# Performance work log

Hardware: AMD Instinct MI355X
Metric: run time of the kernel (lower is better)

## Reference

```python
import jax, jax.numpy as jnp
import numpy as np

N_NODES, F_IN, HID, HEADS, REP, NCLS = 8192, 128, 64, 8, 512, 32
E, NSYN, LMAX = 2048, 4096, 8
DM, DI, DSTATE, DCONV, DTR = 512, 1024, 16, 4, 32


def setup_inputs():
    key = jax.random.key(0)
    ks = jax.random.split(key, 24)
    g = lambda i, shape, s=0.05: jax.random.normal(ks[i], shape, jnp.float32) * s
    return {
        "edge_attr": jax.random.normal(ks[0], (E, 8), jnp.float32),
        "synapse": jax.random.normal(ks[1], (NSYN, 6), jnp.float32),
        "x_param": g(2, (N_NODES, F_IN), 0.1),
        "W1": g(3, (F_IN, HEADS * HID)),
        "att_src1": g(4, (HEADS, HID), 0.1),
        "att_dst1": g(5, (HEADS, HID), 0.1),
        "b1": jnp.zeros((HEADS * HID,), jnp.float32),
        "W2": g(6, (HEADS * HID, REP)),
        "att_src2": g(7, (1, REP), 0.1),
        "att_dst2": g(8, (1, REP), 0.1),
        "b2": jnp.zeros((REP,), jnp.float32),
        "W_in": g(9, (6, DM), 0.1),
        "b_in": jnp.zeros((DM,), jnp.float32),
        "W_inproj": g(10, (DM, 2 * DI)),
        "conv_w": g(11, (DI, DCONV), 0.1),
        "conv_b": jnp.zeros((DI,), jnp.float32),
        "W_xproj": g(12, (DI, DTR + 2 * DSTATE)),
        "W_dt": g(13, (DTR, DI), 0.1),
        "b_dt": jnp.full((DI,), -4.0, jnp.float32),
        "A_log": jnp.log(jnp.tile(jnp.arange(1, DSTATE + 1, dtype=jnp.float32), (DI, 1))),
        "D": jnp.ones((DI,), jnp.float32),
        "W_outproj": g(14, (DI, DM)),
        "W_lout": g(15, (DM, DM)),
        "b_lout": jnp.zeros((DM,), jnp.float32),
        "Wc1": g(16, (REP + 2 * DM, 512)),
        "bc1": jnp.zeros((512,), jnp.float32),
        "Wc2": g(17, (512, NCLS)),
        "bc2": jnp.zeros((NCLS,), jnp.float32),
        "edge_index": jax.random.randint(ks[18], (2, E), 0, N_NODES),
        "synapse_index": jnp.sort(jax.random.randint(ks[19], (NSYN,), 0, E)),
        "scatter_size": N_NODES,
    }


def _gat(x, W, a_src, a_dst, bias, src, dst, heads, out_ch, concat):
    # PyG GATConv (eval mode, edge_dim=None, self-loops already appended to src/dst)
    n = x.shape[0]
    xw = (x @ W).reshape(n, heads, out_ch)
    e = (xw * a_src).sum(-1)[src] + (xw * a_dst).sum(-1)[dst]  # [E+N, H]
    e = jax.nn.leaky_relu(e, 0.2)
    m = jax.ops.segment_max(e, dst, num_segments=n)
    ex = jnp.exp(e - m[dst])
    denom = jax.ops.segment_sum(ex, dst, num_segments=n)
    alpha = ex / denom[dst]
    out = jax.ops.segment_sum(alpha[:, :, None] * xw[src], dst, num_segments=n)
    out = out.reshape(n, heads * out_ch) if concat else out.mean(1)
    return out + bias


def _mamba_encoder(synapse, synapse_index, W_in, b_in, W_inproj, conv_w, conv_b,
                   W_xproj, W_dt, b_dt, A_log, D, W_outproj, W_lout, b_lout):
    # ragged [NSYN,6] -> padded [E, LMAX, 6] (synapse_index is sorted)
    counts = jax.ops.segment_sum(jnp.ones((NSYN,), jnp.int32), synapse_index, num_segments=E)
    starts = jnp.cumsum(counts) - counts
    pos = jnp.arange(NSYN) - starts[synapse_index]
    padded = jnp.zeros((E, LMAX, synapse.shape[1]), synapse.dtype).at[
        synapse_index, pos].set(synapse, mode="drop")
    u = padded @ W_in + b_in                     # linear_in: [E, L, DM]
    xz = u @ W_inproj                            # in_proj:   [E, L, 2*DI]
    xm, z = xz[..., :DI], xz[..., DI:]
    # depthwise causal conv over time
    xc = jax.lax.conv_general_dilated(
        xm.transpose(0, 2, 1), conv_w[:, None, :],
        window_strides=(1,), padding=[(DCONV - 1, 0)],
        dimension_numbers=("NCH", "OIH", "NCH"), feature_group_count=DI)
    xc = jax.nn.silu(xc + conv_b[:, None]).transpose(0, 2, 1)  # [E, L, DI]
    xdb = xc @ W_xproj
    dt = jax.nn.softplus(xdb[..., :DTR] @ W_dt + b_dt)         # [E, L, DI]
    Bm = xdb[..., DTR:DTR + DSTATE]                            # [E, L, N]
    Cm = xdb[..., DTR + DSTATE:]                               # [E, L, N]
    A = -jnp.exp(A_log)                                        # [DI, N]

    def step(h, t):
        dt_t, B_t, C_t, x_t = t                                # [E,DI],[E,N],[E,N],[E,DI]
        h = jnp.exp(dt_t[:, :, None] * A) * h + (dt_t * x_t)[:, :, None] * B_t[:, None, :]
        return h, jnp.einsum("bdn,bn->bd", h, C_t)

    h0 = jnp.zeros((E, DI, DSTATE), xc.dtype)
    _, ys = jax.lax.scan(step, h0, (dt.transpose(1, 0, 2), Bm.transpose(1, 0, 2),
                                    Cm.transpose(1, 0, 2), xc.transpose(1, 0, 2)))
    y = ys.transpose(1, 0, 2) + D * xc                         # [E, L, DI]
    out = (y * jax.nn.silu(z)) @ W_outproj                     # [E, L, DM]
    # masked mean over true sequence length (empty groups behave like a zero seq of len 1)
    cnt = jnp.clip(counts, 1, LMAX).astype(out.dtype)
    mask = (jnp.arange(LMAX)[None, :] < cnt[:, None]).astype(out.dtype)
    pooled = (out * mask[:, :, None]).sum(1) / cnt[:, None]
    return pooled @ W_lout + b_lout                            # [E, DM]


def _forward(edge_attr, synapse, x_param, W1, att_src1, att_dst1, b1,
             W2, att_src2, att_dst2, b2, W_in, b_in, W_inproj, conv_w, conv_b,
             W_xproj, W_dt, b_dt, A_log, D, W_outproj, W_lout, b_lout,
             Wc1, bc1, Wc2, bc2, edge_index, synapse_index, scatter_size):
    # GAT stack (eval: dropouts identity; edge_attr unused since edge_dim=None)
    loops = jnp.arange(N_NODES)
    src = jnp.concatenate([edge_index[0], loops])
    dst = jnp.concatenate([edge_index[1], loops])
    h = jax.nn.elu(_gat(x_param, W1, att_src1, att_dst1, b1, src, dst, HEADS, HID, True))
    h = _gat(h, W2, att_src2, att_dst2, b2, src, dst, 1, REP, False)   # [N, REP]
    x_point = _mamba_encoder(synapse, synapse_index, W_in, b_in, W_inproj, conv_w,
                             conv_b, W_xproj, W_dt, b_dt, A_log, D, W_outproj,
                             W_lout, b_lout)                            # [E, DM]

    def smax(idx):
        s = jax.ops.segment_max(x_point, idx, num_segments=scatter_size)
        nz = jax.ops.segment_sum(jnp.ones((E,), jnp.int32), idx, num_segments=scatter_size)
        return jnp.where(nz[:, None] > 0, s, 0.0)  # torch_scatter: empty slots -> 0

    left, right = smax(edge_index[0]), smax(edge_index[1])
    feats = jnp.concatenate([h, left, right], axis=1)          # [N, REP+2*DM]
    return jax.nn.relu(feats @ Wc1 + bc1) @ Wc2 + bc2          # [N, NCLS]


def reference(edge_attr, synapse, x_param, W1, att_src1, att_dst1, b1,
              W2, att_src2, att_dst2, b2, W_in, b_in, W_inproj, conv_w, conv_b,
              W_xproj, W_dt, b_dt, A_log, D, W_outproj, W_lout, b_lout,
              Wc1, bc1, Wc2, bc2, edge_index, synapse_index, scatter_size):
    return _forward(edge_attr, synapse, x_param, W1, att_src1, att_dst1, b1,
                    W2, att_src2, att_dst2, b2, W_in, b_in, W_inproj, conv_w, conv_b,
                    W_xproj, W_dt, b_dt, A_log, D, W_outproj, W_lout, b_lout,
                    Wc1, bc1, Wc2, bc2, edge_index, synapse_index, scatter_size)
```

## Files before the change

### kernel.cpp

```cpp
#include <hip/hip_runtime.h>

#define N_NODES 8192
#define F_IN 128
#define HID 64
#define HEADS 8
#define REP 512
#define NCLS 32
#define E_EDGES 2048
#define NSYN 4096
#define LMAX 8
#define DM 512
#define DI 1024
#define DSTATE 16
#define DCONV 4
#define DTR 32
#define TOT_EDGES (E_EDGES + N_NODES)
#define ROWS (E_EDGES * LMAX)
#define MC_CAP 6144

typedef short bf16x8 __attribute__((ext_vector_type(8)));
typedef float f32x4 __attribute__((ext_vector_type(4)));

__device__ __forceinline__ unsigned mapf(float f) {
  unsigned u = __float_as_uint(f);
  return (u & 0x80000000u) ? ~u : (u | 0x80000000u);
}
__device__ __forceinline__ float unmapf(unsigned u) {
  return __uint_as_float((u & 0x80000000u) ? (u ^ 0x80000000u) : ~u);
}
__device__ __forceinline__ float fsig(float x) {
  return __builtin_amdgcn_rcpf(1.0f + __expf(-x));
}
__device__ __forceinline__ float fsoftplus(float x) {
  return fmaxf(x, 0.0f) + __logf(1.0f + __expf(-fabsf(x)));
}
__device__ __forceinline__ unsigned short f2bf(float f) {
  unsigned u = __float_as_uint(f);
  unsigned r = (u + 0x7FFFu + ((u >> 16) & 1u)) >> 16;
  return (unsigned short)r;
}
__device__ __forceinline__ float bf2f(unsigned short h) {
  return __uint_as_float(((unsigned)h) << 16);
}
__device__ __forceinline__ void split2(float x, unsigned short* hh, unsigned short* ll) {
  unsigned short h = f2bf(x);
  *hh = h;
  *ll = f2bf(x - bf2f(h));
}
__device__ __forceinline__ int lower_bound_dev(const int* __restrict__ arr, int n, int v) {
  int lo = 0, hi = n;
  while (lo < hi) { int mid = (lo + hi) >> 1; if (arr[mid] < v) lo = mid + 1; else hi = mid; }
  return lo;
}
__device__ __forceinline__ int src_of(const int* __restrict__ ei, int i) {
  return i < E_EDGES ? ei[i] : i - E_EDGES;
}
__device__ __forceinline__ int dst_of(const int* __restrict__ ei, int i) {
  return i < E_EDGES ? ei[E_EDGES + i] : i - E_EDGES;
}
__device__ __forceinline__ int clip_cnt(int c) { return c < 1 ? 1 : (c > LMAX ? LMAX : c); }

__global__ __launch_bounds__(512) void gemm_mfma2(
    const unsigned short* __restrict__ Ah, const unsigned short* __restrict__ Al,
    const unsigned short* __restrict__ Bth, const unsigned short* __restrict__ Btl,
    float* __restrict__ C, int M, int N, int K,
    const float* __restrict__ bias, int act) {
  __shared__ __align__(16) unsigned short As[2][128][40];
  __shared__ __align__(16) unsigned short Bs[2][128][40];
  const int tid = threadIdx.x;
  const int w = tid >> 6;
  const int lane = tid & 63;
  const int wr = w >> 2, wc = w & 3;
  const int mb = M >> 7;
  const int lin = blockIdx.x;
  const int bx = lin / mb;
  const int by = lin % mb;
  const int brow = by * 128;
  const int bcol = bx * 128;
  const int r0 = lane & 15;
  const int kg = lane >> 4;
  const int row0 = tid >> 2, kc0 = tid & 3;
  const size_t a0 = (size_t)(brow + row0) * K + kc0 * 8;
  const size_t b0 = (size_t)(bcol + row0) * K + kc0 * 8;
  f32x4 acc[4][2] = {};
  {
    bf16x8 t0 = *(const bf16x8*)(Ah + a0), t1 = *(const bf16x8*)(Al + a0);
    bf16x8 t2 = *(const bf16x8*)(Bth + b0), t3 = *(const bf16x8*)(Btl + b0);
    *(bf16x8*)(&As[0][row0][kc0 * 8]) = t0;
    *(bf16x8*)(&As[1][row0][kc0 * 8]) = t1;
    *(bf16x8*)(&Bs[0][row0][kc0 * 8]) = t2;
    *(bf16x8*)(&Bs[1][row0][kc0 * 8]) = t3;
  }
  __syncthreads();
  for (int kt = 0; kt < K; kt += 32) {
    const bool more = (kt + 32) < K;
    bf16x8 p0, p1, p2, p3;
    if (more) {
      p0 = *(const bf16x8*)(Ah + a0 + kt + 32);
      p1 = *(const bf16x8*)(Al + a0 + kt + 32);
      p2 = *(const bf16x8*)(Bth + b0 + kt + 32);
      p3 = *(const bf16x8*)(Btl + b0 + kt + 32);
    }
    bf16x8 bhv[2], blv[2];
#pragma unroll
    for (int cf = 0; cf < 2; ++cf) {
      bhv[cf] = *(const bf16x8*)(&Bs[0][wc * 32 + cf * 16 + r0][kg * 8]);
      blv[cf] = *(const bf16x8*)(&Bs[1][wc * 32 + cf * 16 + r0][kg * 8]);
    }
#pragma unroll
    for (int rf = 0; rf < 4; ++rf) {
      bf16x8 ah = *(const bf16x8*)(&As[0][wr * 64 + rf * 16 + r0][kg * 8]);
      bf16x8 al = *(const bf16x8*)(&As[1][wr * 64 + rf * 16 + r0][kg * 8]);
#pragma unroll
      for (int cf = 0; cf < 2; ++cf) {
        acc[rf][cf] = __builtin_amdgcn_mfma_f32_16x16x32_bf16(ah, bhv[cf], acc[rf][cf], 0, 0, 0);
        acc[rf][cf] = __builtin_amdgcn_mfma_f32_16x16x32_bf16(ah, blv[cf], acc[rf][cf], 0, 0, 0);
        acc[rf][cf] = __builtin_amdgcn_mfma_f32_16x16x32_bf16(al, bhv[cf], acc[rf][cf], 0, 0, 0);
      }
    }
    __syncthreads();
    if (more) {
      *(bf16x8*)(&As[0][row0][kc0 * 8]) = p0;
      *(bf16x8*)(&As[1][row0][kc0 * 8]) = p1;
      *(bf16x8*)(&Bs[0][row0][kc0 * 8]) = p2;
      *(bf16x8*)(&Bs[1][row0][kc0 * 8]) = p3;
    }
    __syncthreads();
  }
#pragma unroll
  for (int rf = 0; rf < 4; ++rf)
#pragma unroll
    for (int cf = 0; cf < 2; ++cf) {
      int col = bcol + wc * 32 + cf * 16 + r0;
      float bb = bias ? bias[col] : 0.0f;
#pragma unroll
      for (int j = 0; j < 4; ++j) {
        int row = brow + wr * 64 + rf * 16 + kg * 4 + j;
        float v = acc[rf][cf][j] + bb;
        if (act == 1) v = fmaxf(v, 0.0f);
        C[(size_t)row * N + col] = v;
      }
    }
}

__global__ __launch_bounds__(256) void gemm_mfma_sk(
    const unsigned short* __restrict__ Ah, const unsigned short* __restrict__ Al,
    const unsigned short* __restrict__ Bth, const unsigned short* __restrict__ Btl,
    float* __restrict__ C, int M, int N, int K) {
  __shared__ __align__(16) unsigned short As[2][64][40];
  const int tid = threadIdx.x;
  const int w = tid >> 6;
  const int lane = tid & 63;
  const int brow = blockIdx.y * 64;
  const int bcol = blockIdx.x * 64;
  const int srow = tid >> 2;
  const int skc = tid & 3;
  const int r0 = lane & 15;
  const int kg = lane >> 4;
  const int kchunk = K / gridDim.z;
  const int k0 = blockIdx.z * kchunk;
  f32x4 acc[4] = {};
  const size_t aoff = (size_t)(brow + srow) * K;
  const size_t boff = (size_t)(bcol + w * 16 + r0) * K + kg * 8;
  for (int kt = k0; kt < k0 + kchunk; kt += 32) {
    bf16x8 bh = *(const bf16x8*)(Bth + boff + kt);
    bf16x8 bl = *(const bf16x8*)(Btl + boff + kt);
    *(bf16x8*)(&As[0][srow][skc * 8]) = *(const bf16x8*)(Ah + aoff + kt + skc * 8);
    *(bf16x8*)(&As[1][srow][skc * 8]) = *(const bf16x8*)(Al + aoff + kt + skc * 8);
    __syncthreads();
#pragma unroll
    for (int r = 0; r < 4; ++r) {
      bf16x8 ah = *(const bf16x8*)(&As[0][r * 16 + r0][kg * 8]);
      bf16x8 al = *(const bf16x8*)(&As[1][r * 16 + r0][kg * 8]);
      acc[r] = __builtin_amdgcn_mfma_f32_16x16x32_bf16(ah, bh, acc[r], 0, 0, 0);
      acc[r] = __builtin_amdgcn_mfma_f32_16x16x32_bf16(ah, bl, acc[r], 0, 0, 0);
      acc[r] = __builtin_amdgcn_mfma_f32_16x16x32_bf16(al, bh, acc[r], 0, 0, 0);
    }
    __syncthreads();
  }
  const int col = bcol + w * 16 + r0;
#pragma unroll
  for (int r = 0; r < 4; ++r) {
#pragma unroll
    for (int j = 0; j < 4; ++j) {
      int row = brow + r * 16 + kg * 4 + j;
      atomicAdd(&C[(size_t)row * N + col], acc[r][j]);
    }
  }
}

__global__ __launch_bounds__(256) void gemm_thin32(
    const float* __restrict__ A32,
    const unsigned short* __restrict__ Bth, const unsigned short* __restrict__ Btl,
    float* __restrict__ C, int M, const float* __restrict__ bias) {
  const int tid = threadIdx.x;
  const int w = tid >> 6;
  const int lane = tid & 63;
  const int r0 = lane & 15;
  const int kg = lane >> 4;
  const int rowbase = blockIdx.x * 64 + w * 16;
  f32x4 acc[2] = {};
  const float* arow = A32 + (size_t)(rowbase + r0) * 512 + kg * 8;
  for (int kt = 0; kt < 512; kt += 32) {
    float4 f0 = *(const float4*)(arow + kt);
    float4 f1 = *(const float4*)(arow + kt + 4);
    float v[8] = {f0.x, f0.y, f0.z, f0.w, f1.x, f1.y, f1.z, f1.w};
    bf16x8 ah, al;
#pragma unroll
    for (int j = 0; j < 8; ++j) {
      unsigned short hh, ll;
      split2(v[j], &hh, &ll);
      ah[j] = (short)hh;
      al[j] = (short)ll;
    }
#pragma unroll
    for (int cf = 0; cf < 2; ++cf) {
      bf16x8 bh = *(const bf16x8*)(Bth + (size_t)(cf * 16 + r0) * 512 + kt + kg * 8);
      bf16x8 bl = *(const bf16x8*)(Btl + (size_t)(cf * 16 + r0) * 512 + kt + kg * 8);
      acc[cf] = __builtin_amdgcn_mfma_f32_16x16x32_bf16(ah, bh, acc[cf], 0, 0, 0);
      acc[cf] = __builtin_amdgcn_mfma_f32_16x16x32_bf16(ah, bl, acc[cf], 0, 0, 0);
      acc[cf] = __builtin_amdgcn_mfma_f32_16x16x32_bf16(al, bh, acc[cf], 0, 0, 0);
    }
  }
#pragma unroll
  for (int cf = 0; cf < 2; ++cf) {
    int col = cf * 16 + r0;
    float bb = bias[col];
#pragma unroll
    for (int j = 0; j < 4; ++j) {
      int row = rowbase + kg * 4 + j;
      C[(size_t)row * 32 + col] = acc[cf][j] + bb;
    }
  }
}

__global__ void split_kernel(const float* __restrict__ x, unsigned short* __restrict__ h,
                             unsigned short* __restrict__ l, int n) {
  int i = blockIdx.x * 256 + threadIdx.x;
  if (i >= n) return;
  split2(x[i], &h[i], &l[i]);
}

__global__ void tsplit_kernel(const float* __restrict__ W, unsigned short* __restrict__ Wth,
                              unsigned short* __restrict__ Wtl, int K, int N) {
  int i = blockIdx.x * 256 + threadIdx.x;
  if (i >= K * N) return;
  int k = i / N, n = i - k * N;
  float v = W[i];
  unsigned short h = f2bf(v);
  Wth[(size_t)n * K + k] = h;
  Wtl[(size_t)n * K + k] = f2bf(v - bf2f(h));
}

template <int BM, int BN>
__global__ __launch_bounds__(256) void gemm_t(
    const float* __restrict__ A, int lda,
    const float* __restrict__ B, int ldb,
    float* __restrict__ C, int ldc,
    int M, int N, int K,
    const float* __restrict__ bias, int act) {
  constexpr int RR = BM / 64;
  constexpr int CR = BN / 64;
  __shared__ float As[16][BM + 4];
  __shared__ float Bs[16][BN + 4];
  const int tid = threadIdx.x;
  const int tx = tid & 15;
  const int ty = tid >> 4;
  const int brow = blockIdx.y * BM;
  const int bcol = blockIdx.x * BN;
  float acc[RR][CR][4][4] = {};
  for (int kt = 0; kt < K; kt += 16) {
#pragma unroll
    for (int p = 0; p < RR; ++p) {
      int c = tid + p * 256;
      int row = c >> 2, kc = c & 3;
      int gr = brow + row;
      float4 v = make_float4(0.f, 0.f, 0.f, 0.f);
      if (gr < M) v = *reinterpret_cast<const float4*>(A + (size_t)gr * lda + kt + kc * 4);
      As[kc * 4 + 0][row] = v.x;
      As[kc * 4 + 1][row] = v.y;
      As[kc * 4 + 2][row] = v.z;
      As[kc * 4 + 3][row] = v.w;
    }
#pragma unroll
    for (int p = 0; p < CR; ++p) {
      int c = tid + p * 256;
      int k = c / (BN / 4), c4 = c % (BN / 4);
      int gc = bcol + c4 * 4;
      float4 v = make_float4(0.f, 0.f, 0.f, 0.f);
      if (gc < N) v = *reinterpret_cast<const float4*>(B + (size_t)(kt + k) * ldb + gc);
      *reinterpret_cast<float4*>(&Bs[k][c4 * 4]) = v;
    }
    __syncthreads();
#pragma unroll
    for (int k = 0; k < 16; ++k) {
      float av[RR * 4], bv[CR * 4];
#pragma unroll
      for (int r = 0; r < RR; ++r) {
        float4 t = *reinterpret_cast<const float4*>(&As[k][r * 64 + ty * 4]);
        av[r * 4 + 0] = t.x; av[r * 4 + 1] = t.y; av[r * 4 + 2] = t.z; av[r * 4 + 3] = t.w;
      }
#pragma unroll
      for (int cq = 0; cq < CR; ++cq) {
        float4 t = *reinterpret_cast<const float4*>(&Bs[k][cq * 64 + tx * 4]);
        bv[cq * 4 + 0] = t.x; bv[cq * 4 + 1] = t.y; bv[cq * 4 + 2] = t.z; bv[cq * 4 + 3] = t.w;
      }
#pragma unroll
      for (int r = 0; r < RR; ++r)
#pragma unroll
        for (int cq = 0; cq < CR; ++cq)
#pragma unroll
          for (int i = 0; i < 4; ++i)
#pragma unroll
            for (int j = 0; j < 4; ++j)
              acc[r][cq][i][j] = fmaf(av[r * 4 + i], bv[cq * 4 + j], acc[r][cq][i][j]);
    }
    __syncthreads();
  }
#pragma unroll
  for (int r = 0; r < RR; ++r)
#pragma unroll
    for (int i = 0; i < 4; ++i) {
      int row = brow + r * 64 + ty * 4 + i;
      if (row >= M) continue;
#pragma unroll
      for (int cq = 0; cq < CR; ++cq) {
        int col = bcol + cq * 64 + tx * 4;
        if (col >= N) continue;
        float4 v;
        v.x = acc[r][cq][i][0]; v.y = acc[r][cq][i][1];
        v.z = acc[r][cq][i][2]; v.w = acc[r][cq][i][3];
        if (bias) {
          float4 bb = *reinterpret_cast<const float4*>(bias + col);
          v.x += bb.x; v.y += bb.y; v.z += bb.z; v.w += bb.w;
        }
        if (act == 1) {
          v.x = fmaxf(v.x, 0.f); v.y = fmaxf(v.y, 0.f);
          v.z = fmaxf(v.z, 0.f); v.w = fmaxf(v.w, 0.f);
        }
        *reinterpret_cast<float4*>(C + (size_t)row * ldc + col) = v;
      }
    }
}

__global__ void counts_kernel(const int* __restrict__ sidx, int* __restrict__ counts) {
  int e = blockIdx.x * 256 + threadIdx.x;
  if (e >= E_EDGES) return;
  int lo = lower_bound_dev(sidx, NSYN, e);
  int hi = lower_bound_dev(sidx, NSYN, e + 1);
  counts[e] = hi - lo;
}

__global__ void scatter_padded_kernel(const float* __restrict__ synapse,
                                      const int* __restrict__ sidx,
                                      float* __restrict__ padded) {
  int i = blockIdx.x * 256 + threadIdx.x;
  if (i >= NSYN) return;
  int e = sidx[i];
  int lo = lower_bound_dev(sidx, NSYN, e);
  int pos = i - lo;
  if (pos < LMAX) {
#pragma unroll
    for (int c = 0; c < 6; ++c) padded[((size_t)e * LMAX + pos) * 6 + c] = synapse[(size_t)i * 6 + c];
  }
}

__global__ __launch_bounds__(256) void prefix_kernel(const int* __restrict__ counts,
                                                     int* __restrict__ starts_c) {
  __shared__ int part[256];
  int t = threadIdx.x;
  int loc[8];
  int s = 0;
#pragma unroll
  for (int i = 0; i < 8; ++i) {
    int c = clip_cnt(counts[t * 8 + i]);
    loc[i] = s;
    s += c;
  }
  part[t] = s;
  __syncthreads();
  int mytot = s;
  for (int o = 1; o < 256; o <<= 1) {
    int add = (t >= o) ? part[t - o] : 0;
    __syncthreads();
    part[t] += add;
    __syncthreads();
  }
  int off = part[t] - mytot;
#pragma unroll
  for (int i = 0; i < 8; ++i) starts_c[t * 8 + i] = off + loc[i];
}

__global__ __launch_bounds__(256) void xc_compact_kernel(
    const float* __restrict__ padded,
    const float* __restrict__ W_eff, const float* __restrict__ b_eff,
    const float* __restrict__ conv_w, const float* __restrict__ conv_b,
    const int* __restrict__ counts, const int* __restrict__ starts_c,
    unsigned short* __restrict__ xch, unsigned short* __restrict__ xcl) {
  __shared__ float pads[LMAX * 6];
  int t = threadIdx.x;
  int d = blockIdx.x * 256 + t;
  int e = blockIdx.y;
  if (t < LMAX * 6) pads[t] = padded[(size_t)e * LMAX * 6 + t];
  __syncthreads();
  int cnt = clip_cnt(counts[e]);
  int sc = starts_c[e];
  float wef[6];
#pragma unroll
  for (int c = 0; c < 6; ++c) wef[c] = W_eff[c * 2048 + d];
  float cw0 = conv_w[d * 4 + 0], cw1 = conv_w[d * 4 + 1];
  float cw2 = conv_w[d * 4 + 2], cw3 = conv_w[d * 4 + 3];
  float cb = conv_b[d], be = b_eff[d];
  float x0 = 0.f, x1 = 0.f, x2 = 0.f;
  for (int l = 0; l < cnt; ++l) {
    float xm = be;
#pragma unroll
    for (int c = 0; c < 6; ++c) xm += pads[l * 6 + c] * wef[c];
    float s0 = cb + xm * cw3;
    if (l >= 1) s0 += x2 * cw2;
    if (l >= 2) s0 += x1 * cw1;
    if (l >= 3) s0 += x0 * cw0;
    float v = s0 * fsig(s0);
    size_t o = (size_t)(sc + l) * DI + d;
    split2(v, &xch[o], &xcl[o]);
    x0 = x1; x1 = x2; x2 = xm;
  }
}

__global__ __launch_bounds__(256) void mamba_scan_pool_kernel(
    const float* __restrict__ xdb_c, const float* __restrict__ padded,
    const float* __restrict__ W_eff, const float* __restrict__ b_eff,
    const float* __restrict__ W_dt, const float* __restrict__ b_dt,
    const float* __restrict__ A_log, const float* __restrict__ Dv,
    const float* __restrict__ conv_w, const float* __restrict__ conv_b,
    const int* __restrict__ counts, const int* __restrict__ starts_c,
    unsigned short* __restrict__ pooledh, unsigned short* __restrict__ pooledl) {
  __shared__ float pads[LMAX * 6];
  int t = threadIdx.x;
  int d = blockIdx.x * 256 + t;
  int e = blockIdx.y;
  if (t < LMAX * 6) pads[t] = padded[(size_t)e * LMAX * 6 + t];
  float wdt[DTR];
#pragma unroll
  for (int k = 0; k < DTR; ++k) wdt[k] = W_dt[k * DI + d];
  float a[DSTATE];
#pragma unroll
  for (int n = 0; n < DSTATE; ++n) a[n] = -__expf(A_log[d * DSTATE + n]);
  float h[DSTATE];
#pragma unroll
  for (int n = 0; n < DSTATE; ++n) h[n] = 0.0f;
  float wef[6], wez[6];
#pragma unroll
  for (int c = 0; c < 6; ++c) {
    wef[c] = W_eff[c * 2048 + d];
    wez[c] = W_eff[c * 2048 + DI + d];
  }
  float cw0 = conv_w[d * 4 + 0], cw1 = conv_w[d * 4 + 1];
  float cw2 = conv_w[d * 4 + 2], cw3 = conv_w[d * 4 + 3];
  float cb = conv_b[d];
  float bdt = b_dt[d], Dd = Dv[d], be = b_eff[d], bez = b_eff[DI + d];
  __syncthreads();
  int cnt = clip_cnt(counts[e]);
  int sc = starts_c[e];
  float x0 = 0.f, x1 = 0.f, x2 = 0.f;
  float ssum = 0.0f;
  for (int l = 0; l < cnt; ++l) {
    float xm = be;
#pragma unroll
    for (int c = 0; c < 6; ++c) xm += pads[l * 6 + c] * wef[c];
    float s0 = cb + xm * cw3;
    if (l >= 1) s0 += x2 * cw2;
    if (l >= 2) s0 += x1 * cw1;
    if (l >= 3) s0 += x0 * cw0;
    float xt = s0 * fsig(s0);
    const float* __restrict__ xrow = xdb_c + (size_t)(sc + l) * 64;
    float acc = bdt;
#pragma unroll
    for (int k = 0; k < DTR; ++k) acc += xrow[k] * wdt[k];
    float dt = fsoftplus(acc);
    float dtx = dt * xt;
    float y = 0.0f;
#pragma unroll
    for (int n = 0; n < DSTATE; ++n) {
      float en = __expf(dt * a[n]);
      h[n] = en * h[n] + dtx * xrow[32 + n];
      y += h[n] * xrow[48 + n];
    }
    y += Dd * xt;
    float z = bez;
#pragma unroll
    for (int c = 0; c < 6; ++c) z += pads[l * 6 + c] * wez[c];
    ssum += y * z * fsig(z);
    x0 = x1; x1 = x2; x2 = xm;
  }
  float pv = ssum / (float)cnt;
  split2(pv, &pooledh[(size_t)e * DI + d], &pooledl[(size_t)e * DI + d]);
}

__global__ void esed1_kernel(const float* __restrict__ xw1, const float* __restrict__ as1,
                             const float* __restrict__ ad1, float* __restrict__ es1,
                             float* __restrict__ ed1) {
  int idx = blockIdx.x * 256 + threadIdx.x;
  int n = idx >> 3, h = idx & 7;
  const float* xr = xw1 + (size_t)n * 512 + h * 64;
  const float* sr = as1 + h * 64;
  const float* dr = ad1 + h * 64;
  float es = 0.0f, ed = 0.0f;
#pragma unroll
  for (int c = 0; c < 64; ++c) { float v = xr[c]; es += v * sr[c]; ed += v * dr[c]; }
  es1[idx] = es; ed1[idx] = ed;
}

__global__ void edge1_kernel(const int* __restrict__ ei, const float* __restrict__ es1,
                             const float* __restrict__ ed1, float* __restrict__ e1,
                             unsigned* __restrict__ m1u) {
  int idx = blockIdx.x * 256 + threadIdx.x;
  if (idx >= TOT_EDGES * HEADS) return;
  int i = idx >> 3, h = idx & 7;
  int s = src_of(ei, i), d = dst_of(ei, i);
  float v = es1[s * 8 + h] + ed1[d * 8 + h];
  v = v >= 0.0f ? v : 0.2f * v;
  e1[idx] = v;
  atomicMax(m1u + d * 8 + h, mapf(v));
}

__global__ void ex1_kernel(const int* __restrict__ ei, float* __restrict__ e1,
                           const unsigned* __restrict__ m1u, float* __restrict__ denom1) {
  int idx = blockIdx.x * 256 + threadIdx.x;
  if (idx >= TOT_EDGES * HEADS) return;
  int i = idx >> 3, h = idx & 7;
  int d = dst_of(ei, i);
  float ex = expf(e1[idx] - unmapf(m1u[d * 8 + h]));
  e1[idx] = ex;
  atomicAdd(denom1 + d * 8 + h, ex);
}

__global__ void selfinit1_kernel(const float* __restrict__ e1, const float* __restrict__ denom1,
                                 const float* __restrict__ xw1, float* __restrict__ g1) {
  int idx = blockIdx.x * 256 + threadIdx.x;
  int n = idx >> 9, j = idx & 511;
  int h = j >> 6;
  float alpha = e1[(size_t)(E_EDGES + n) * 8 + h] / denom1[n * 8 + h];
  g1[idx] = alpha * xw1[idx];
}

__global__ __launch_bounds__(256) void agg1_kernel(const int* __restrict__ ei,
                                                   const float* __restrict__ e1,
                                                   const float* __restrict__ denom1,
                                                   const float* __restrict__ xw1,
                                                   float* __restrict__ g1) {
  int i = blockIdx.x;
  int s = ei[i], d = ei[E_EDGES + i];
  for (int j = threadIdx.x; j < 512; j += 256) {
    int h = j >> 6;
    float alpha = e1[i * 8 + h] / denom1[d * 8 + h];
    atomicAdd(g1 + (size_t)d * 512 + j, alpha * xw1[(size_t)s * 512 + j]);
  }
}

__global__ void elu_bias_split_kernel(const float* __restrict__ g1, const float* __restrict__ b1,
                                      unsigned short* __restrict__ g1h,
                                      unsigned short* __restrict__ g1l) {
  int idx = blockIdx.x * 256 + threadIdx.x;
  int j = idx & 511;
  float v = g1[idx] + b1[j];
  v = v > 0.0f ? v : expm1f(v);
  split2(v, &g1h[idx], &g1l[idx]);
}

__global__ __launch_bounds__(64) void esed2_kernel(const float* __restrict__ xw2,
                                                   const float* __restrict__ as2,
                                                   const float* __restrict__ ad2,
                                                   float* __restrict__ es2,
                                                   float* __restrict__ ed2) {
  int n = blockIdx.x, t = threadIdx.x;
  float es = 0.0f, ed = 0.0f;
  for (int c = t; c < 512; c += 64) {
    float v = xw2[(size_t)n * 512 + c];
    es += v * as2[c]; ed += v * ad2[c];
  }
#pragma unroll
  for (int o = 32; o > 0; o >>= 1) { es += __shfl_down(es, o, 64); ed += __shfl_down(ed, o, 64); }
  if (t == 0) { es2[n] = es; ed2[n] = ed; }
}

__global__ void edge2_kernel(const int* __restrict__ ei, const float* __restrict__ es2,
                             const float* __restrict__ ed2, float* __restrict__ e2,
                             unsigned* __restrict__ m2u) {
  int i = blockIdx.x * 256 + threadIdx.x;
  if (i >= TOT_EDGES) return;
  int s = src_of(ei, i), d = dst_of(ei, i);
  float v = es2[s] + ed2[d];
  v = v >= 0.0f ? v : 0.2f * v;
  e2[i] = v;
  atomicMax(m2u + d, mapf(v));
}

__global__ void ex2_kernel(const int* __restrict__ ei, float* __restrict__ e2,
                           const unsigned* __restrict__ m2u, float* __restrict__ denom2) {
  int i = blockIdx.x * 256 + threadIdx.x;
  if (i >= TOT_EDGES) return;
  int d = dst_of(ei, i);
  float ex = expf(e2[i] - unmapf(m2u[d]));
  e2[i] = ex;
  atomicAdd(denom2 + d, ex);
}

__global__ void selfinit2_kernel(const float* __restrict__ e2, const float* __restrict__ denom2,
                                 const float* __restrict__ xw2, float* __restrict__ g2) {
  int idx = blockIdx.x * 256 + threadIdx.x;
  int n = idx >> 9;
  float alpha = e2[E_EDGES + n] / denom2[n];
  g2[idx] = alpha * xw2[idx];
}

__global__ __launch_bounds__(256) void agg2_kernel(const int* __restrict__ ei,
                                                   const float* __restrict__ e2,
                                                   const float* __restrict__ denom2,
                                                   const float* __restrict__ xw2,
                                                   float* __restrict__ g2) {
  int i = blockIdx.x;
  int s = ei[i], d = ei[E_EDGES + i];
  float alpha = e2[i] / denom2[d];
  for (int j = threadIdx.x; j < 512; j += 256) {
    atomicAdd(g2 + (size_t)d * 512 + j, alpha * xw2[(size_t)s * 512 + j]);
  }
}

__global__ __launch_bounds__(256) void leftright_kernel(const int* __restrict__ ei,
                                                        const float* __restrict__ xp,
                                                        const float* __restrict__ b_lout,
                                                        unsigned* __restrict__ leftU,
                                                        unsigned* __restrict__ rightU,
                                                        int* __restrict__ flagL,
                                                        int* __restrict__ flagR) {
  int i = blockIdx.x;
  int s = ei[i], d = ei[E_EDGES + i];
  if (threadIdx.x == 0) { flagL[s] = 1; flagR[d] = 1; }
  for (int j = threadIdx.x; j < 512; j += 256) {
    unsigned v = mapf(xp[(size_t)i * 512 + j] + b_lout[j]);
    atomicMax(leftU + (size_t)s * 512 + j, v);
    atomicMax(rightU + (size_t)d * 512 + j, v);
  }
}

__global__ void concat_split_kernel(const float* __restrict__ g2, const float* __restrict__ b2,
                                    const unsigned* __restrict__ leftU,
                                    const unsigned* __restrict__ rightU,
                                    const int* __restrict__ flagL, const int* __restrict__ flagR,
                                    unsigned short* __restrict__ fh,
                                    unsigned short* __restrict__ fl) {
  int idx = blockIdx.x * 256 + threadIdx.x;
  int n = idx >> 9, j = idx & 511;
  size_t base = (size_t)n * 1536 + j;
  split2(g2[idx] + b2[j], &fh[base], &fl[base]);
  split2(flagL[n] ? unmapf(leftU[idx]) : 0.0f, &fh[base + 512], &fl[base + 512]);
  split2(flagR[n] ? unmapf(rightU[idx]) : 0.0f, &fh[base + 1024], &fl[base + 1024]);
}

extern "C" void kernel_launch(void* const* d_in, const int* in_sizes, int n_in,
                              void* d_out, int out_size, void* d_ws, size_t ws_size,
                              hipStream_t stream) {
  const float* synapse = (const float*)d_in[1];
  const float* x_param = (const float*)d_in[2];
  const float* W1 = (const float*)d_in[3];
  const float* as1 = (const float*)d_in[4];
  const float* ad1 = (const float*)d_in[5];
  const float* b1 = (const float*)d_in[6];
  const float* W2 = (const float*)d_in[7];
  const float* as2 = (const float*)d_in[8];
  const float* ad2 = (const float*)d_in[9];
  const float* b2 = (const float*)d_in[10];
  const float* W_in = (const float*)d_in[11];
  const float* b_in = (const float*)d_in[12];
  const float* W_inproj = (const float*)d_in[13];
  const float* conv_w = (const float*)d_in[14];
  const float* conv_b = (const float*)d_in[15];
  const float* W_xproj = (const float*)d_in[16];
  const float* W_dt = (const float*)d_in[17];
  const float* b_dt = (const float*)d_in[18];
  const float* A_log = (const float*)d_in[19];
  const float* Dv = (const float*)d_in[20];
  const float* W_outproj = (const float*)d_in[21];
  const float* W_lout = (const float*)d_in[22];
  const float* b_lout = (const float*)d_in[23];
  const float* Wc1 = (const float*)d_in[24];
  const float* bc1 = (const float*)d_in[25];
  const float* Wc2 = (const float*)d_in[26];
  const float* bc2 = (const float*)d_in[27];
  const int* edge_index = (const int*)d_in[28];
  const int* sidx = (const int*)d_in[29];
  float* out = (float*)d_out;

  const size_t MB = (size_t)1 << 20;
  const size_t KB = (size_t)1 << 10;
  char* ws = (char*)d_ws;
  unsigned short* xc_ch = (unsigned short*)(ws + 0);
  unsigned short* xc_cl = (unsigned short*)(ws + 16 * MB);
  float* xw1 = (float*)(ws + 0);
  float* g1 = (float*)(ws + 16 * MB);
  unsigned short* g1h = (unsigned short*)(ws + 32 * MB);
  unsigned short* g1l = (unsigned short*)(ws + 40 * MB);
  unsigned short* xph = (unsigned short*)(ws + 48 * MB);
  unsigned short* xpl = (unsigned short*)(ws + 50 * MB);
  unsigned short* W1th = (unsigned short*)(ws + 52 * MB);
  unsigned short* W1tl = (unsigned short*)(ws + 52 * MB + 128 * KB);
  float* xw2 = (float*)(ws + 48 * MB);
  unsigned short* W2th = (unsigned short*)(ws + 0);
  unsigned short* W2tl = (unsigned short*)(ws + 512 * KB);
  float* g2 = (float*)(ws + 0);
  unsigned short* featsh = (unsigned short*)(ws + 16 * MB);
  unsigned short* featsl = (unsigned short*)(ws + 40 * MB);
  float* hidden = (float*)(ws + 0);
  float* xdb_c = (float*)(ws + 64 * MB);
  unsigned short* pooledh = (unsigned short*)(ws + 68 * MB);
  unsigned short* pooledl = (unsigned short*)(ws + 72 * MB);
  unsigned short* Wxth = (unsigned short*)(ws + 76 * MB);
  unsigned short* Wxtl = (unsigned short*)(ws + 76 * MB + 128 * KB);
  float* WmixT = (float*)(ws + 77 * MB);
  unsigned short* Wmixth = (unsigned short*)(ws + 80 * MB);
  unsigned short* Wmixtl = (unsigned short*)(ws + 81 * MB);
  unsigned short* Wlth = (unsigned short*)(ws + 82 * MB);
  unsigned short* Wltl = (unsigned short*)(ws + 82 * MB + 512 * KB);
  unsigned short* Woph = (unsigned short*)(ws + 83 * MB);
  unsigned short* Wopl = (unsigned short*)(ws + 84 * MB);
  unsigned* leftU = (unsigned*)(ws + 64 * MB);
  unsigned* rightU = (unsigned*)(ws + 80 * MB);
  float* x_point = (float*)(ws + 96 * MB);
  unsigned short* Wc1th = (unsigned short*)(ws + 96 * MB);
  unsigned short* Wc1tl = (unsigned short*)(ws + 96 * MB + 1536 * KB);
  unsigned short* Wc2th = (unsigned short*)(ws + 99 * MB);
  unsigned short* Wc2tl = (unsigned short*)(ws + 99 * MB + 64 * KB);
  char* sm = ws + 100 * MB;
  float* es1 = (float*)(sm + 0);
  float* ed1 = (float*)(sm + 256 * KB);
  float* e1 = (float*)(sm + 512 * KB);
  unsigned* m1u = (unsigned*)(sm + 832 * KB);
  float* denom1 = (float*)(sm + 1088 * KB);
  float* es2 = (float*)(sm + 1344 * KB);
  float* ed2 = (float*)(sm + 1376 * KB);
  float* e2 = (float*)(sm + 1408 * KB);
  unsigned* m2u = (unsigned*)(sm + 1448 * KB);
  float* denom2 = (float*)(sm + 1480 * KB);
  int* flagL = (int*)(sm + 1512 * KB);
  int* flagR = (int*)(sm + 1544 * KB);
  float* padded = (float*)(ws + 106 * MB);
  int* counts = (int*)(ws + 106 * MB + 384 * KB);
  float* W_eff = (float*)(ws + 106 * MB + 400 * KB);
  float* b_eff = (float*)(ws + 106 * MB + 448 * KB);
  int* starts_c = (int*)(ws + 106 * MB + 456 * KB);

  auto g64 = [&](const float* A, int lda, const float* B, int ldb, float* C, int ldc,
                 int M, int N, int K, const float* bias, int act) {
    dim3 grid((N + 63) / 64, (M + 63) / 64);
    gemm_t<64, 64><<<grid, 256, 0, stream>>>(A, lda, B, ldb, C, ldc, M, N, K, bias, act);
  };
  auto gm2 = [&](const unsigned short* Ah, const unsigned short* Al,
                 const unsigned short* Bth, const unsigned short* Btl, float* C,
                 int M, int N, int K, const float* bias, int act) {
    gemm_mfma2<<<(N / 128) * (M / 128), 512, 0, stream>>>(Ah, Al, Bth, Btl, C, M, N, K, bias,
                                                          act);
  };
  auto tsplit = [&](const float* W, unsigned short* th, unsigned short* tl, int K, int N) {
    tsplit_kernel<<<(K * N + 255) / 256, 256, 0, stream>>>(W, th, tl, K, N);
  };
  auto split = [&](const float* x, unsigned short* h, unsigned short* l, int n) {
    split_kernel<<<(n + 255) / 256, 256, 0, stream>>>(x, h, l, n);
  };

  g64(W_in, DM, W_inproj, 2 * DI, W_eff, 2 * DI, 6, 2 * DI, DM, nullptr, 0);
  g64(b_in, DM, W_inproj, 2 * DI, b_eff, 2 * DI, 1, 2 * DI, DM, nullptr, 0);
  tsplit(W_lout, Wlth, Wltl, DM, DM);
  split(W_outproj, Woph, Wopl, DI * DM);
  gm2(Wlth, Wltl, Woph, Wopl, WmixT, DM, DI, DM, nullptr, 0);
  split(WmixT, Wmixth, Wmixtl, DM * DI);

  hipMemsetAsync(padded, 0, (size_t)ROWS * 6 * 4, stream);
  scatter_padded_kernel<<<(NSYN + 255) / 256, 256, 0, stream>>>(synapse, sidx, padded);
  counts_kernel<<<(E_EDGES + 255) / 256, 256, 0, stream>>>(sidx, counts);
  prefix_kernel<<<1, 256, 0, stream>>>(counts, starts_c);
  xc_compact_kernel<<<dim3(DI / 256, E_EDGES), 256, 0, stream>>>(
      padded, W_eff, b_eff, conv_w, conv_b, counts, starts_c, xc_ch, xc_cl);
  tsplit(W_xproj, Wxth, Wxtl, DI, 64);
  hipMemsetAsync(xdb_c, 0, (size_t)MC_CAP * 64 * 4, stream);
  gemm_mfma_sk<<<dim3(1, MC_CAP / 64, 8), 256, 0, stream>>>(xc_ch, xc_cl, Wxth, Wxtl, xdb_c,
                                                            MC_CAP, 64, DI);
  mamba_scan_pool_kernel<<<dim3(DI / 256, E_EDGES), 256, 0, stream>>>(
      xdb_c, padded, W_eff, b_eff, W_dt, b_dt, A_log, Dv, conv_w, conv_b, counts, starts_c,
      pooledh, pooledl);
  hipMemsetAsync(x_point, 0, (size_t)E_EDGES * DM * 4, stream);
  gemm_mfma_sk<<<dim3(DM / 64, E_EDGES / 64, 4), 256, 0, stream>>>(pooledh, pooledl, Wmixth,
                                                                   Wmixtl, x_point, E_EDGES,
                                                                   DM, DI);

  split(x_param, xph, xpl, N_NODES * F_IN);
  tsplit(W1, W1th, W1tl, F_IN, HEADS * HID);
  gm2(xph, xpl, W1th, W1tl, xw1, N_NODES, HEADS * HID, F_IN, nullptr, 0);
  esed1_kernel<<<(N_NODES * HEADS) / 256, 256, 0, stream>>>(xw1, as1, ad1, es1, ed1);
  hipMemsetAsync(m1u, 0, 512 * KB, stream);
  edge1_kernel<<<(TOT_EDGES * HEADS + 255) / 256, 256, 0, stream>>>(edge_index, es1, ed1, e1, m1u);
  ex1_kernel<<<(TOT_EDGES * HEADS + 255) / 256, 256, 0, stream>>>(edge_index, e1, m1u, denom1);
  selfinit1_kernel<<<(N_NODES * 512) / 256, 256, 0, stream>>>(e1, denom1, xw1, g1);
  agg1_kernel<<<E_EDGES, 256, 0, stream>>>(edge_index, e1, denom1, xw1, g1);
  elu_bias_split_kernel<<<(N_NODES * 512) / 256, 256, 0, stream>>>(g1, b1, g1h, g1l);

  tsplit(W2, W2th, W2tl, HEADS * HID, REP);
  gm2(g1h, g1l, W2th, W2tl, xw2, N_NODES, REP, HEADS * HID, nullptr, 0);
  esed2_kernel<<<N_NODES, 64, 0, stream>>>(xw2, as2, ad2, es2, ed2);
  hipMemsetAsync(m2u, 0, 128 * KB, stream);
  edge2_kernel<<<(TOT_EDGES + 255) / 256, 256, 0, stream>>>(edge_index, es2, ed2, e2, m2u);
  ex2_kernel<<<(TOT_EDGES + 255) / 256, 256, 0, stream>>>(edge_index, e2, m2u, denom2);
  selfinit2_kernel<<<(N_NODES * 512) / 256, 256, 0, stream>>>(e2, denom2, xw2, g2);
  agg2_kernel<<<E_EDGES, 256, 0, stream>>>(edge_index, e2, denom2, xw2, g2);

  hipMemsetAsync(leftU, 0, 32 * MB, stream);
  leftright_kernel<<<E_EDGES, 256, 0, stream>>>(edge_index, x_point, b_lout, leftU, rightU,
                                                flagL, flagR);

  concat_split_kernel<<<(N_NODES * 512) / 256, 256, 0, stream>>>(g2, b2, leftU, rightU, flagL,
                                                                 flagR, featsh, featsl);
  tsplit(Wc1, Wc1th, Wc1tl, REP + 2 * DM, 512);
  tsplit(Wc2, Wc2th, Wc2tl, 512, NCLS);
  gm2(featsh, featsl, Wc1th, Wc1tl, hidden, N_NODES, 512, REP + 2 * DM, bc1, 1);
  gemm_thin32<<<N_NODES / 64, 256, 0, stream>>>(hidden, Wc2th, Wc2tl, out, N_NODES, bc2);
}
```

Measured before the change: 427.2 us.

## Process two edges per scan block and use split-K GEMM for weight mix

The Mamba scan/pool kernel now handles two edges per thread block. Per-channel parameters (W_dt, A_log, conv weights, W_eff) are loaded once and reused across both, halving the grid and the redundant parameter loads. The two recurrences are interleaved to add independent work per thread, at the cost of more registers and divergence when counts differ. Separately, the WmixT weight product switches from the 128x128 tile GEMM to the split-K GEMM with a memset, which spreads that small GEMM over more blocks.

```diff
diff --git a/kernel.cpp b/kernel.cpp
--- a/kernel.cpp
+++ b/kernel.cpp
@@ -427,7 +427,7 @@
   }
 }
 
-__global__ __launch_bounds__(256) void mamba_scan_pool_kernel(
+__global__ __launch_bounds__(256) void mamba_scan_pool2_kernel(
     const float* __restrict__ xdb_c, const float* __restrict__ padded,
     const float* __restrict__ W_eff, const float* __restrict__ b_eff,
     const float* __restrict__ W_dt, const float* __restrict__ b_dt,
@@ -435,20 +435,24 @@
     const float* __restrict__ conv_w, const float* __restrict__ conv_b,
     const int* __restrict__ counts, const int* __restrict__ starts_c,
     unsigned short* __restrict__ pooledh, unsigned short* __restrict__ pooledl) {
-  __shared__ float pads[LMAX * 6];
+  __shared__ float pads[2][LMAX * 6];
   int t = threadIdx.x;
   int d = blockIdx.x * 256 + t;
-  int e = blockIdx.y;
-  if (t < LMAX * 6) pads[t] = padded[(size_t)e * LMAX * 6 + t];
+  int e0 = blockIdx.y * 2;
+  int e1 = e0 + 1;
+  if (t < LMAX * 6) {
+    pads[0][t] = padded[(size_t)e0 * LMAX * 6 + t];
+    pads[1][t] = padded[(size_t)e1 * LMAX * 6 + t];
+  }
   float wdt[DTR];
 #pragma unroll
   for (int k = 0; k < DTR; ++k) wdt[k] = W_dt[k * DI + d];
   float a[DSTATE];
 #pragma unroll
   for (int n = 0; n < DSTATE; ++n) a[n] = -__expf(A_log[d * DSTATE + n]);
-  float h[DSTATE];
-#pragma unroll
-  for (int n = 0; n < DSTATE; ++n) h[n] = 0.0f;
+  float h0[DSTATE], h1[DSTATE];
+#pragma unroll
+  for (int n = 0; n < DSTATE; ++n) { h0[n] = 0.0f; h1[n] = 0.0f; }
   float wef[6], wez[6];
 #pragma unroll
   for (int c = 0; c < 6; ++c) {
@@ -460,41 +464,74 @@
   float cb = conv_b[d];
   float bdt = b_dt[d], Dd = Dv[d], be = b_eff[d], bez = b_eff[DI + d];
   __syncthreads();
-  int cnt = clip_cnt(counts[e]);
-  int sc = starts_c[e];
-  float x0 = 0.f, x1 = 0.f, x2 = 0.f;
-  float ssum = 0.0f;
-  for (int l = 0; l < cnt; ++l) {
-    float xm = be;
-#pragma unroll
-    for (int c = 0; c < 6; ++c) xm += pads[l * 6 + c] * wef[c];
-    float s0 = cb + xm * cw3;
-    if (l >= 1) s0 += x2 * cw2;
-    if (l >= 2) s0 += x1 * cw1;
-    if (l >= 3) s0 += x0 * cw0;
-    float xt = s0 * fsig(s0);
-    const float* __restrict__ xrow = xdb_c + (size_t)(sc + l) * 64;
-    float acc = bdt;
-#pragma unroll
-    for (int k = 0; k < DTR; ++k) acc += xrow[k] * wdt[k];
-    float dt = fsoftplus(acc);
-    float dtx = dt * xt;
-    float y = 0.0f;
-#pragma unroll
-    for (int n = 0; n < DSTATE; ++n) {
-      float en = __expf(dt * a[n]);
-      h[n] = en * h[n] + dtx * xrow[32 + n];
-      y += h[n] * xrow[48 + n];
-    }
-    y += Dd * xt;
-    float z = bez;
-#pragma unroll
-    for (int c = 0; c < 6; ++c) z += pads[l * 6 + c] * wez[c];
-    ssum += y * z * fsig(z);
-    x0 = x1; x1 = x2; x2 = xm;
-  }
-  float pv = ssum / (float)cnt;
-  split2(pv, &pooledh[(size_t)e * DI + d], &pooledl[(size_t)e * DI + d]);
+  int cnt0 = clip_cnt(counts[e0]), cnt1 = clip_cnt(counts[e1]);
+  int sc0 = starts_c[e0], sc1 = starts_c[e1];
+  float x00 = 0.f, x01 = 0.f, x02 = 0.f;
+  float x10 = 0.f, x11 = 0.f, x12 = 0.f;
+  float ss0 = 0.0f, ss1 = 0.0f;
+  int cmax = cnt0 > cnt1 ? cnt0 : cnt1;
+  for (int l = 0; l < cmax; ++l) {
+    if (l < cnt0) {
+      float xm = be;
+#pragma unroll
+      for (int c = 0; c < 6; ++c) xm += pads[0][l * 6 + c] * wef[c];
+      float s0 = cb + xm * cw3;
+      if (l >= 1) s0 += x02 * cw2;
+      if (l >= 2) s0 += x01 * cw1;
+      if (l >= 3) s0 += x00 * cw0;
+      float xt = s0 * fsig(s0);
+      const float* __restrict__ xrow = xdb_c + (size_t)(sc0 + l) * 64;
+      float acc = bdt;
+#pragma unroll
+      for (int k = 0; k < DTR; ++k) acc += xrow[k] * wdt[k];
+      float dt = fsoftplus(acc);
+      float dtx = dt * xt;
+      float y = 0.0f;
+#pragma unroll
+      for (int n = 0; n < DSTATE; ++n) {
+        float en = __expf(dt * a[n]);
+        h0[n] = en * h0[n] + dtx * xrow[32 + n];
+        y += h0[n] * xrow[48 + n];
+      }
+      y += Dd * xt;
+      float z = bez;
+#pragma unroll
+      for (int c = 0; c < 6; ++c) z += pads[0][l * 6 + c] * wez[c];
+      ss0 += y * z * fsig(z);
+      x00 = x01; x01 = x02; x02 = xm;
+    }
+    if (l < cnt1) {
+      float xm = be;
+#pragma unroll
+      for (int c = 0; c < 6; ++c) xm += pads[1][l * 6 + c] * wef[c];
+      float s0 = cb + xm * cw3;
+      if (l >= 1) s0 += x12 * cw2;
+      if (l >= 2) s0 += x11 * cw1;
+      if (l >= 3) s0 += x10 * cw0;
+      float xt = s0 * fsig(s0);
+      const float* __restrict__ xrow = xdb_c + (size_t)(sc1 + l) * 64;
+      float acc = bdt;
+#pragma unroll
+      for (int k = 0; k < DTR; ++k) acc += xrow[k] * wdt[k];
+      float dt = fsoftplus(acc);
+      float dtx = dt * xt;
+      float y = 0.0f;
+#pragma unroll
+      for (int n = 0; n < DSTATE; ++n) {
+        float en = __expf(dt * a[n]);
+        h1[n] = en * h1[n] + dtx * xrow[32 + n];
+        y += h1[n] * xrow[48 + n];
+      }
+      y += Dd * xt;
+      float z = bez;
+#pragma unroll
+      for (int c = 0; c < 6; ++c) z += pads[1][l * 6 + c] * wez[c];
+      ss1 += y * z * fsig(z);
+      x10 = x11; x11 = x12; x12 = xm;
+    }
+  }
+  split2(ss0 / (float)cnt0, &pooledh[(size_t)e0 * DI + d], &pooledl[(size_t)e0 * DI + d]);
+  split2(ss1 / (float)cnt1, &pooledh[(size_t)e1 * DI + d], &pooledl[(size_t)e1 * DI + d]);
 }
 
 __global__ void esed1_kernel(const float* __restrict__ xw1, const float* __restrict__ as1,
@@ -772,7 +809,9 @@
   g64(b_in, DM, W_inproj, 2 * DI, b_eff, 2 * DI, 1, 2 * DI, DM, nullptr, 0);
   tsplit(W_lout, Wlth, Wltl, DM, DM);
   split(W_outproj, Woph, Wopl, DI * DM);
-  gm2(Wlth, Wltl, Woph, Wopl, WmixT, DM, DI, DM, nullptr, 0);
+  hipMemsetAsync(WmixT, 0, (size_t)DM * DI * 4, stream);
+  gemm_mfma_sk<<<dim3(DI / 64, DM / 64, 4), 256, 0, stream>>>(Wlth, Wltl, Woph, Wopl, WmixT,
+                                                              DM, DI, DM);
   split(WmixT, Wmixth, Wmixtl, DM * DI);
 
   hipMemsetAsync(padded, 0, (size_t)ROWS * 6 * 4, stream);
@@ -785,7 +824,7 @@
   hipMemsetAsync(xdb_c, 0, (size_t)MC_CAP * 64 * 4, stream);
   gemm_mfma_sk<<<dim3(1, MC_CAP / 64, 8), 256, 0, stream>>>(xc_ch, xc_cl, Wxth, Wxtl, xdb_c,
                                                             MC_CAP, 64, DI);
-  mamba_scan_pool_kernel<<<dim3(DI / 256, E_EDGES), 256, 0, stream>>>(
+  mamba_scan_pool2_kernel<<<dim3(DI / 256, E_EDGES / 2), 256, 0, stream>>>(
       xdb_c, padded, W_eff, b_eff, W_dt, b_dt, A_log, Dv, conv_w, conv_b, counts, starts_c,
       pooledh, pooledl);
   hipMemsetAsync(x_point, 0, (size_t)E_EDGES * DM * 4, stream);
```

Result: no change. 425.7 us (-0.4%).
